# Optimization experiments

Measured on AMD Instinct MI355X. Metric: run time of the kernel, lower is better.

The kernel has to match this reference:

```python
import jax, jax.numpy as jnp
import numpy as np

B, S, E = 2, 2048, 2048
H, HKV = 16, 4
G = H // HKV
QLR, KVLR = 1024, 512
DN, DR, DV = 128, 64, 128
DQK = DN + DR
EPS = 1.1920929e-07  # torch.finfo(float32).eps, F.rms_norm default


def rms_norm(x):
    return x * jax.lax.rsqrt(jnp.mean(x * x, axis=-1, keepdims=True) + EPS)


def apply_rope(x, cos, sin):
    # x: [B, S, h, D]; pairs are adjacent elements (torch view_as_complex convention)
    x0, x1 = x[..., 0::2], x[..., 1::2]            # [B,S,h,D/2]
    c = cos[None, :, None, :]
    s = sin[None, :, None, :]
    r0 = x0 * c - x1 * s
    r1 = x0 * s + x1 * c
    return jnp.stack([r0, r1], axis=-1).reshape(x.shape)


def setup_inputs() -> dict:
    key = jax.random.key(0)
    ks = jax.random.split(key, 8)
    inv_freq = 1.0 / (10000.0 ** (np.arange(0, DR, 2, dtype=np.float32) / DR))  # [DR/2]
    ang = np.arange(S, dtype=np.float32)[:, None] * inv_freq[None, :]           # [S, DR/2]
    return {
        "x": jax.random.normal(ks[0], (B, S, E), jnp.float32),
        "freqs_cos": jnp.asarray(np.cos(ang), jnp.float32),
        "freqs_sin": jnp.asarray(np.sin(ang), jnp.float32),
        "Wqa": jax.random.normal(ks[1], (QLR, E), jnp.float32) * (E ** -0.5),
        "Wqb": jax.random.normal(ks[2], (H * DQK, QLR), jnp.float32) * (QLR ** -0.5),
        "Wkva": jax.random.normal(ks[3], (KVLR + DR, E), jnp.float32) * (E ** -0.5),
        "Wkvb": jax.random.normal(ks[4], (HKV * (DN + DV), KVLR), jnp.float32) * (KVLR ** -0.5),
        "Wo": jax.random.normal(ks[5], (E, H * DV), jnp.float32) * ((H * DV) ** -0.5),
    }


def reference(x, freqs_cos, freqs_sin, Wqa, Wqb, Wkva, Wkvb, Wo):
    # Q path: low-rank down-proj -> rmsnorm -> up-proj
    q = rms_norm(x @ Wqa.T) @ Wqb.T                       # [B,S,H*DQK]
    q = q.reshape(B, S, H, DQK)
    q_nope, q_rope = q[..., :DN], q[..., DN:]
    q_rope = apply_rope(q_rope, freqs_cos, freqs_sin)
    q = jnp.concatenate([q_nope, q_rope], axis=-1)        # [B,S,H,DQK]

    # KV path: joint down-proj, shared rope key, up-proj of latent
    kv_a = x @ Wkva.T                                     # [B,S,KVLR+DR]
    kv_latent, k_rope = kv_a[..., :KVLR], kv_a[..., KVLR:]
    k_rope = jnp.broadcast_to(k_rope[:, :, None, :], (B, S, HKV, DR))
    k_rope = apply_rope(k_rope, freqs_cos, freqs_sin)     # [B,S,HKV,DR]
    kv = (rms_norm(kv_latent) @ Wkvb.T).reshape(B, S, HKV, DN + DV)
    k_nope, v = kv[..., :DN], kv[..., DN:]
    k = jnp.concatenate([k_nope, k_rope], axis=-1)        # [B,S,HKV,DQK]

    # GQA causal SDPA: group G query heads per kv head
    qg = q.reshape(B, S, HKV, G, DQK)
    scores = jnp.einsum("bsngd,btnd->bngst", qg, k) * (DQK ** -0.5)  # [B,HKV,G,S,S]
    causal = jnp.tril(jnp.ones((S, S), bool))
    scores = jnp.where(causal, scores, jnp.finfo(scores.dtype).min)
    attn = jax.nn.softmax(scores, axis=-1)
    o = jnp.einsum("bngst,btnd->bsngd", attn, v).reshape(B, S, H * DV)
    return o @ Wo.T                                        # [B,S,E]
```

## Files before the change

### kernel.cpp

```cpp
#include <hip/hip_runtime.h>
#include <cstdint>
#include <cstddef>

typedef __attribute__((ext_vector_type(4))) float f32x4;
typedef __attribute__((ext_vector_type(2))) float f32x2;
typedef __attribute__((ext_vector_type(8))) short short8;
typedef __attribute__((ext_vector_type(8))) __bf16 bf16x8;
typedef unsigned short u16;
typedef unsigned int u32;
typedef __attribute__((ext_vector_type(2))) unsigned int u32x2;
typedef __attribute__((ext_vector_type(4))) unsigned short u16x4;
typedef __attribute__((ext_vector_type(2))) unsigned short u16x2;

#define EPS_RMS 1.1920929e-07f

__device__ __forceinline__ u16 f2bf(float f) {
  union { float f; unsigned u; } v; v.f = f;
  unsigned r = v.u + 0x7FFFu + ((v.u >> 16) & 1u);
  return (u16)(r >> 16);
}
__device__ __forceinline__ float b2f(u16 x) {
  union { unsigned u; float f; } v; v.u = ((unsigned)x) << 16;
  return v.f;
}
__device__ __forceinline__ u32 cvt_pk_bf16(float lo, float hi) {
  u32 r;
  asm("v_cvt_pk_bf16_f32 %0, %1, %2" : "=v"(r) : "v"(lo), "v"(hi));
  return r;
}

template <typename V>
__device__ __forceinline__ auto mfma_try(V a, V b, f32x4 c, int)
    -> decltype(__builtin_amdgcn_mfma_f32_16x16x32_bf16(a, b, c, 0, 0, 0)) {
  return __builtin_amdgcn_mfma_f32_16x16x32_bf16(a, b, c, 0, 0, 0);
}
template <typename V>
__device__ __forceinline__ f32x4 mfma_try(V a, V b, f32x4 c, long) {
  return __builtin_amdgcn_mfma_f32_16x16x32_bf16(
      __builtin_bit_cast(bf16x8, a), __builtin_bit_cast(bf16x8, b), c, 0, 0, 0);
}
__device__ __forceinline__ f32x4 mfma_bf16(short8 a, short8 b, f32x4 c) {
  return mfma_try(a, b, c, 0);
}

__device__ __forceinline__ void load_lds16(u16* lds, const u16* g) {
  auto* gp = reinterpret_cast<const __attribute__((address_space(1))) unsigned int*>(
      reinterpret_cast<uintptr_t>(g));
  auto* lp = reinterpret_cast<__attribute__((address_space(3))) unsigned int*>(
      reinterpret_cast<uintptr_t>(lds));
  __builtin_amdgcn_global_load_lds(gp, lp, 16, 0, 0);
}

__device__ __forceinline__ float fast_exp2(float x) {
  return __builtin_amdgcn_exp2f(x);
}

template <int CTRL>
__device__ __forceinline__ float dpp_step(float v) {
  int t = __builtin_amdgcn_update_dpp(0, __builtin_bit_cast(int, v), CTRL, 0xF, 0xF, true);
  return __builtin_bit_cast(float, t);
}

__global__ __launch_bounds__(256) void cvt_all(const float* __restrict__ x,
                                               const float* __restrict__ Wqa,
                                               const float* __restrict__ Wkva,
                                               const float* __restrict__ Wqb,
                                               const float* __restrict__ Wkvb,
                                               const float* __restrict__ Wo,
                                               u16* __restrict__ xb,
                                               u16* __restrict__ wacat,
                                               u16* __restrict__ wqb,
                                               u16* __restrict__ wkvb,
                                               u16* __restrict__ wo) {
  const int blk = blockIdx.x;
  if (blk >= 8192 && blk < 11520) {
    int i = (blk - 8192) * 256 + threadIdx.x;
    int r = i >> 9;
    int c4 = i & 511;
    f32x4 v = {0.f, 0.f, 0.f, 0.f};
    if (r < 1024) v = ((const f32x4*)Wqa)[r * 512 + c4];
    else if (r < 1600) v = ((const f32x4*)Wkva)[(r - 1024) * 512 + c4];
    u16x4 o = {f2bf(v.x), f2bf(v.y), f2bf(v.z), f2bf(v.w)};
    ((u16x4*)wacat)[i] = o;
    return;
  }
  const float* src;
  u16* dst;
  int i;
  if (blk < 8192)       { i = blk * 256 + threadIdx.x;           src = x;    dst = xb;   }
  else if (blk < 14592) { i = (blk - 11520) * 256 + threadIdx.x; src = Wqb;  dst = wqb;  }
  else if (blk < 15104) { i = (blk - 14592) * 256 + threadIdx.x; src = Wkvb; dst = wkvb; }
  else                  { i = (blk - 15104) * 256 + threadIdx.x; src = Wo;   dst = wo;   }
  f32x4 v = ((const f32x4*)src)[i];
  u16x4 o = {f2bf(v.x), f2bf(v.y), f2bf(v.z), f2bf(v.w)};
  ((u16x4*)dst)[i] = o;
}

template <typename OutT, int EPI>
__global__ __launch_bounds__(256) void gemm_bt(const u16* __restrict__ A,
                                               const u16* __restrict__ B,
                                               OutT* __restrict__ C,
                                               int M, int N, int K, int gx,
                                               const float* __restrict__ fc,
                                               const float* __restrict__ fs,
                                               u16* __restrict__ aux) {
  __shared__ __align__(16) u16 As[2][128 * 64];
  __shared__ __align__(16) u16 Bs[2][128 * 64];
  const int nwg = gridDim.x;
  const int cpx = nwg >> 3;
  const int swz = (blockIdx.x & 7) * cpx + (blockIdx.x >> 3);
  const int by = swz / gx, bxx = swz - by * gx;
  const int tid = threadIdx.x;
  const int lane = tid & 63, w = tid >> 6;
  const int wr = w >> 1, wc = w & 1;
  const int l16 = lane & 15, lg = lane >> 4;
  const int row0 = by * 128, col0 = bxx * 128;

  const u16* Ab = A + (size_t)row0 * K;
  const u16* Bb = B + (size_t)col0 * K;

  f32x4 acc[4][4] = {};

  int soff[4], ldst[4];
#pragma unroll
  for (int j = 0; j < 4; ++j) {
    int c = j * 256 + tid;
    int row = c >> 3;
    int rb = (c & 7) << 4;
    int sb = rb ^ ((row & 7) << 4);
    soff[j] = row * K + (sb >> 1);
    ldst[j] = c * 8;
  }

#pragma unroll
  for (int j = 0; j < 4; ++j) load_lds16(As[0] + ldst[j], Ab + soff[j]);
#pragma unroll
  for (int j = 0; j < 4; ++j) load_lds16(Bs[0] + ldst[j], Bb + soff[j]);
  __syncthreads();

  int cur = 0;
  for (int k0 = 0; k0 < K; k0 += 64) {
    if (k0 + 64 < K) {
#pragma unroll
      for (int j = 0; j < 4; ++j) load_lds16(As[cur ^ 1] + ldst[j], Ab + soff[j] + k0 + 64);
#pragma unroll
      for (int j = 0; j < 4; ++j) load_lds16(Bs[cur ^ 1] + ldst[j], Bb + soff[j] + k0 + 64);
    }
    const u16* Ac = As[cur];
    const u16* Bc = Bs[cur];
    short8 a[2][4], bfr[2][4];
#pragma unroll
    for (int mt = 0; mt < 4; ++mt) {
      const int rowA = wr * 64 + mt * 16 + l16;
      const int sw = (rowA & 7) << 4;
#pragma unroll
      for (int kk = 0; kk < 2; ++kk)
        a[kk][mt] = *(const short8*)(Ac + rowA * 64 + (((kk * 64 + lg * 16) ^ sw) >> 1));
    }
#pragma unroll
    for (int nt = 0; nt < 4; ++nt) {
      const int rowB = wc * 64 + nt * 16 + l16;
      const int sw = (rowB & 7) << 4;
#pragma unroll
      for (int kk = 0; kk < 2; ++kk)
        bfr[kk][nt] = *(const short8*)(Bc + rowB * 64 + (((kk * 64 + lg * 16) ^ sw) >> 1));
    }
#pragma unroll
    for (int kk = 0; kk < 2; ++kk)
#pragma unroll
      for (int mt = 0; mt < 4; ++mt)
#pragma unroll
        for (int nt = 0; nt < 4; ++nt)
          acc[mt][nt] = mfma_bf16(a[kk][mt], bfr[kk][nt], acc[mt][nt]);
    __syncthreads();
    cur ^= 1;
  }

  if constexpr (EPI == 0 || EPI == 1) {
#pragma unroll
    for (int mt = 0; mt < 4; ++mt)
#pragma unroll
      for (int nt = 0; nt < 4; ++nt)
#pragma unroll
        for (int i = 0; i < 4; ++i) {
          int row = row0 + wr * 64 + mt * 16 + lg * 4 + i;
          int col = col0 + wc * 64 + nt * 16 + l16;
          if constexpr (EPI == 0)
            C[(size_t)row * N + col] = acc[mt][nt][i];
          else
            C[(size_t)row * N + col] = f2bf(acc[mt][nt][i]);
        }
  } else if constexpr (EPI == 2) {
    const float qscale = 0.07216878364870322f * 1.4426950408889634f;
#pragma unroll
    for (int mt = 0; mt < 4; ++mt)
#pragma unroll
      for (int nt = 0; nt < 4; ++nt) {
        int col = col0 + wc * 64 + nt * 16 + l16;
        int hh = ((col >> 6) * 43) >> 7;
        int cin = col - hh * 192;
        int m = (cin - 128) >> 1;
#pragma unroll
        for (int i = 0; i < 4; ++i) {
          int row = row0 + wr * 64 + mt * 16 + lg * 4 + i;
          int bb = row >> 11, ss = row & 2047;
          float v = acc[mt][nt][i];
          float pv = dpp_step<0xB1>(v);
          float val = v;
          if (cin >= 128) {
            float c = fc[ss * 32 + m], sn = fs[ss * 32 + m];
            val = ((l16 & 1) == 0) ? (v * c - pv * sn) : (pv * sn + v * c);
          }
          ((u16*)C)[((size_t)((bb * 16 + hh) * 2048 + ss)) * 192 + cin] = f2bf(val * qscale);
        }
      }
  } else {
#pragma unroll
    for (int mt = 0; mt < 4; ++mt)
#pragma unroll
      for (int nt = 0; nt < 4; ++nt) {
        int col = col0 + wc * 64 + nt * 16 + l16;
        int nn = col >> 8, cin = col & 255;
        int rowb = row0 + wr * 64 + mt * 16 + lg * 4;
        int bb = rowb >> 11, ss0 = rowb & 2047;
        if (cin < 128) {
#pragma unroll
          for (int i = 0; i < 4; ++i)
            ((u16*)C)[((size_t)((bb * 4 + nn) * 2048 + ss0 + i)) * 192 + cin] =
                f2bf(acc[mt][nt][i]);
        } else {
          int dv = cin - 128;
          u16x4 o = {f2bf(acc[mt][nt][0]), f2bf(acc[mt][nt][1]),
                     f2bf(acc[mt][nt][2]), f2bf(acc[mt][nt][3])};
          *(u16x4*)(aux + ((size_t)((bb * 4 + nn) * 128 + dv)) * 2048 + ss0) = o;
        }
      }
  }
}

__global__ __launch_bounds__(256) void rms_fused(const u16* __restrict__ c1b,
                                                 const float* __restrict__ fc,
                                                 const float* __restrict__ fs,
                                                 u16* __restrict__ qlat,
                                                 u16* __restrict__ kvlat,
                                                 u16* __restrict__ Ka) {
  __shared__ float smq[4], smk[4];
  int t = blockIdx.x;
  const u16* row = c1b + (size_t)t * 1664;
  u16x4 v4u = ((const u16x4*)row)[threadIdx.x];
  u16x2 v2u = ((const u16x2*)(row + 1024))[threadIdx.x];
  float v4x = b2f(v4u.x), v4y = b2f(v4u.y), v4z = b2f(v4u.z), v4w = b2f(v4u.w);
  float v2x = b2f(v2u.x), v2y = b2f(v2u.y);
  float sq = v4x * v4x + v4y * v4y + v4z * v4z + v4w * v4w;
  float sk = v2x * v2x + v2y * v2y;
#pragma unroll
  for (int off = 32; off; off >>= 1) { sq += __shfl_xor(sq, off); sk += __shfl_xor(sk, off); }
  if ((threadIdx.x & 63) == 0) { smq[threadIdx.x >> 6] = sq; smk[threadIdx.x >> 6] = sk; }
  __syncthreads();
  float rq = rsqrtf((smq[0] + smq[1] + smq[2] + smq[3]) * (1.0f / 1024.0f) + EPS_RMS);
  float rk = rsqrtf((smk[0] + smk[1] + smk[2] + smk[3]) * (1.0f / 512.0f) + EPS_RMS);
  u16x4 oq = {f2bf(v4x * rq), f2bf(v4y * rq), f2bf(v4z * rq), f2bf(v4w * rq)};
  ((u16x4*)(qlat + (size_t)t * 1024))[threadIdx.x] = oq;
  u16x2 ok = {f2bf(v2x * rk), f2bf(v2y * rk)};
  ((u16x2*)(kvlat + (size_t)t * 512))[threadIdx.x] = ok;
  if (threadIdx.x < 32) {
    int bb = t >> 11, s = t & 2047;
    int m = threadIdx.x;
    float x0 = b2f(row[1536 + 2 * m]), x1 = b2f(row[1537 + 2 * m]);
    float c = fc[s * 32 + m], sn = fs[s * 32 + m];
    u16 r0 = f2bf(x0 * c - x1 * sn);
    u16 r1 = f2bf(x0 * sn + x1 * c);
#pragma unroll
    for (int nn = 0; nn < 4; ++nn) {
      size_t base = ((size_t)((bb * 4 + nn) * 2048 + s)) * 192 + 128;
      Ka[base + 2 * m] = r0;
      Ka[base + 2 * m + 1] = r1;
    }
  }
}

__global__ __launch_bounds__(256, 2) void attn_kernel(const u16* __restrict__ Qa,
                                                      const u16* __restrict__ Ka,
                                                      const u16* __restrict__ VTp,
                                                      u16* __restrict__ Ob) {
  __shared__ __align__(16) u16 Ks[64 * 192];
  __shared__ __align__(16) u16 Vs[128 * 64];
  __shared__ __align__(16) u32 Ppk[4][32][36];
  const int gid = blockIdx.x;
  const int bx = (gid < 256) ? (15 - (gid >> 5)) : ((gid - 256) >> 5);
  const int hb = gid & 31;
  const int b = hb >> 4;
  const int h = hb & 15;
  const int n = h >> 2;
  const int tid = threadIdx.x;
  const int lane = tid & 63;
  const int w = tid >> 6;
  const int l16 = lane & 15;
  const int lg = lane >> 4;

  const u16* Qp = Qa + ((size_t)((b * 16 + h) * 2048 + bx * 128 + w * 32)) * 192;
  const u16* Kp = Ka + ((size_t)((b * 4 + n) * 2048)) * 192;
  const u16* Vp = VTp + ((size_t)((b * 4 + n) * 128)) * 2048;

  int oK[6];
#pragma unroll
  for (int j = 0; j < 6; ++j) {
    int c = j * 256 + tid;
    int row = (c * 2731) >> 16;
    int rb = (c - row * 24) << 4;
    int sb = rb ^ ((row & 7) << 4);
    oK[j] = row * 192 + (sb >> 1);
  }
  int oV[4];
#pragma unroll
  for (int j = 0; j < 4; ++j) {
    int c = j * 256 + tid;
    int row = c >> 3;
    int rb = (c & 7) << 4;
    int sb = rb ^ ((row & 7) << 4);
    oV[j] = row * 2048 + (sb >> 1);
  }

  short8 qf[2][6];
#pragma unroll
  for (int g = 0; g < 2; ++g)
#pragma unroll
    for (int kc = 0; kc < 6; ++kc)
      qf[g][kc] = *(const short8*)(Qp + (size_t)(g * 16 + l16) * 192 + kc * 32 + lg * 8);

  float mrow[2], lrow[2];
  f32x4 oacc[2][8];
#pragma unroll
  for (int g = 0; g < 2; ++g) { mrow[g] = -1e30f; lrow[g] = 0.f; }
#pragma unroll
  for (int g = 0; g < 2; ++g)
#pragma unroll
    for (int vb = 0; vb < 8; ++vb) oacc[g][vb] = (f32x4){0.f, 0.f, 0.f, 0.f};

  const int wrow = bx * 128 + w * 32;
  const int NT = 2 * bx + 2;

  f32x4 kreg[6], vreg[4];
#pragma unroll
  for (int j = 0; j < 6; ++j) kreg[j] = *(const f32x4*)(Kp + oK[j]);
#pragma unroll
  for (int j = 0; j < 4; ++j) vreg[j] = *(const f32x4*)(Vp + oV[j]);

  for (int kt = 0; kt < NT; ++kt) {
    const int kb = kt * 64;
    __syncthreads();
#pragma unroll
    for (int j = 0; j < 6; ++j) *(f32x4*)(Ks + (j * 256 + tid) * 8) = kreg[j];
#pragma unroll
    for (int j = 0; j < 4; ++j) *(f32x4*)(Vs + (j * 256 + tid) * 8) = vreg[j];
    __syncthreads();
    if (kt + 1 < NT) {
      const int kb2 = kb + 64;
#pragma unroll
      for (int j = 0; j < 6; ++j)
        kreg[j] = *(const f32x4*)(Kp + oK[j] + (size_t)kb2 * 192);
#pragma unroll
      for (int j = 0; j < 4; ++j)
        vreg[j] = *(const f32x4*)(Vp + oV[j] + kb2);
    }
    if (kb > wrow + 31) continue;

    f32x4 sc[2][4];
#pragma unroll
    for (int g = 0; g < 2; ++g)
#pragma unroll
      for (int kn = 0; kn < 4; ++kn) sc[g][kn] = (f32x4){0.f, 0.f, 0.f, 0.f};
    __builtin_amdgcn_s_setprio(1);
#pragma unroll
    for (int kn = 0; kn < 4; ++kn) {
      const int rk = kn * 16 + l16;
      const u16* kbase = Ks + rk * 192;
      const int sw = (rk & 7) << 4;
#pragma unroll
      for (int kc = 0; kc < 6; ++kc) {
        short8 kf = *(const short8*)(kbase + (((kc * 64 + lg * 16) ^ sw) >> 1));
        sc[0][kn] = mfma_bf16(kf, qf[0][kc], sc[0][kn]);
        sc[1][kn] = mfma_bf16(kf, qf[1][kc], sc[1][kn]);
      }
    }
    __builtin_amdgcn_s_setprio(0);
    if (kb + 63 > wrow) {
#pragma unroll
      for (int g = 0; g < 2; ++g) {
        const int qabs = wrow + g * 16 + l16;
#pragma unroll
        for (int kn = 0; kn < 4; ++kn)
#pragma unroll
          for (int i = 0; i < 4; ++i)
            if (kb + kn * 16 + lg * 4 + i > qabs) sc[g][kn][i] = -1e30f;
      }
    }
    float pmax[2];
    int need = 0;
#pragma unroll
    for (int g = 0; g < 2; ++g) {
      float v = -1e30f;
#pragma unroll
      for (int kn = 0; kn < 4; ++kn)
        v = fmaxf(v, fmaxf(fmaxf(sc[g][kn][0], sc[g][kn][1]),
                           fmaxf(sc[g][kn][2], sc[g][kn][3])));
      v = fmaxf(v, __shfl_xor(v, 16));
      v = fmaxf(v, __shfl_xor(v, 32));
      pmax[g] = v;
      need |= (v > mrow[g] + 8.0f) ? 1 : 0;
    }
    if (__any(need)) {
#pragma unroll
      for (int g = 0; g < 2; ++g) {
        float mn = fmaxf(mrow[g], pmax[g]);
        float al = fast_exp2(mrow[g] - mn);
        mrow[g] = mn;
        lrow[g] *= al;
#pragma unroll
        for (int i = 0; i < 4; ++i) {
          float alq = __shfl(al, lg * 4 + i);
#pragma unroll
          for (int vb = 0; vb < 8; ++vb) oacc[g][vb][i] *= alq;
        }
      }
    }
#pragma unroll
    for (int g = 0; g < 2; ++g) {
      float rs = 0.f;
#pragma unroll
      for (int kn = 0; kn < 4; ++kn)
#pragma unroll
        for (int i = 0; i < 4; ++i) {
          float p = fast_exp2(sc[g][kn][i] - mrow[g]);
          sc[g][kn][i] = p;
          rs += p;
        }
      rs += __shfl_xor(rs, 16);
      rs += __shfl_xor(rs, 32);
      lrow[g] += rs;
    }
#pragma unroll
    for (int g = 0; g < 2; ++g) {
      const int r = g * 16 + l16;
#pragma unroll
      for (int kn = 0; kn < 4; ++kn) {
        u32x2 pk = {cvt_pk_bf16(sc[g][kn][0], sc[g][kn][1]),
                    cvt_pk_bf16(sc[g][kn][2], sc[g][kn][3])};
        *(u32x2*)&Ppk[w][r][kn * 8 + 2 * lg] = pk;
      }
    }
    short8 pa[2][2];
#pragma unroll
    for (int g = 0; g < 2; ++g) {
      const int r = g * 16 + l16;
      pa[g][0] = *(const short8*)&Ppk[w][r][lg * 4];
      pa[g][1] = *(const short8*)&Ppk[w][r][16 + lg * 4];
    }
    __builtin_amdgcn_s_setprio(1);
#pragma unroll
    for (int vb = 0; vb < 8; ++vb) {
      const int rv = vb * 16 + l16;
      const u16* vbase = Vs + rv * 64;
      const int swv = (rv & 7) << 4;
      short8 v0 = *(const short8*)(vbase + (((lg * 16) ^ swv) >> 1));
      short8 v1 = *(const short8*)(vbase + (((64 + lg * 16) ^ swv) >> 1));
      oacc[0][vb] = mfma_bf16(pa[0][0], v0, oacc[0][vb]);
      oacc[1][vb] = mfma_bf16(pa[1][0], v0, oacc[1][vb]);
      oacc[0][vb] = mfma_bf16(pa[0][1], v1, oacc[0][vb]);
      oacc[1][vb] = mfma_bf16(pa[1][1], v1, oacc[1][vb]);
    }
    __builtin_amdgcn_s_setprio(0);
  }
#pragma unroll
  for (int g = 0; g < 2; ++g) {
    float inv = 1.0f / lrow[g];
#pragma unroll
    for (int i = 0; i < 4; ++i) {
      float invq = __shfl(inv, lg * 4 + i);
      int srow = wrow + g * 16 + lg * 4 + i;
      size_t base = ((size_t)(b * 2048 + srow)) * 2048 + h * 128;
#pragma unroll
      for (int vb = 0; vb < 8; ++vb)
        Ob[base + vb * 16 + l16] = f2bf(oacc[g][vb][i] * invq);
    }
  }
}

extern "C" void kernel_launch(void* const* d_in, const int* in_sizes, int n_in,
                              void* d_out, int out_size, void* d_ws, size_t ws_size,
                              hipStream_t stream) {
  const float* x = (const float*)d_in[0];
  const float* fc = (const float*)d_in[1];
  const float* fs = (const float*)d_in[2];
  const float* Wqa = (const float*)d_in[3];
  const float* Wqb = (const float*)d_in[4];
  const float* Wkva = (const float*)d_in[5];
  const float* Wkvb = (const float*)d_in[6];
  const float* Wo = (const float*)d_in[7];
  float* out = (float*)d_out;

  char* ws = (char*)d_ws;
  u16* xb    = (u16*)(ws + 0);
  u16* wacat = (u16*)(ws + 16777216);
  u16* wqb   = (u16*)(ws + 23592960);
  u16* wkvb  = (u16*)(ws + 29884416);
  u16* wo    = (u16*)(ws + 30932992);
  u16* c1b   = (u16*)(ws + 39321600);
  u16* qlat  = (u16*)(ws + 52953088);
  u16* kvlat = (u16*)(ws + 61341696);
  u16* obf   = (u16*)(ws + 65536000);
  u16* qattn = (u16*)(ws + 82313216);
  u16* kattn = (u16*)(ws + 107479040);
  u16* vt    = (u16*)(ws + 113770496);
  if (ws_size < 117964800u) return;

  cvt_all<<<19200, 256, 0, stream>>>(x, Wqa, Wkva, Wqb, Wkvb, Wo,
                                     xb, wacat, wqb, wkvb, wo);

  gemm_bt<u16, 1><<<416, 256, 0, stream>>>(xb, wacat, c1b, 4096, 1664, 2048, 13,
                                           nullptr, nullptr, nullptr);
  rms_fused<<<4096, 256, 0, stream>>>(c1b, fc, fs, qlat, kvlat, kattn);
  gemm_bt<u16, 2><<<768, 256, 0, stream>>>(qlat, wqb, qattn, 4096, 3072, 1024, 24,
                                           fc, fs, nullptr);
  gemm_bt<u16, 3><<<256, 256, 0, stream>>>(kvlat, wkvb, kattn, 4096, 1024, 512, 8,
                                           nullptr, nullptr, vt);
  attn_kernel<<<512, 256, 0, stream>>>(qattn, kattn, vt, obf);
  gemm_bt<float, 0><<<512, 256, 0, stream>>>(obf, wo, out, 4096, 2048, 2048, 16,
                                             nullptr, nullptr, nullptr);
}
```

Baseline: 238.0 us.

## Double-buffer K/V tiles in LDS and drop to one barrier per iteration

```diff
diff --git a/kernel.cpp b/kernel.cpp
--- a/kernel.cpp
+++ b/kernel.cpp
@@ -283,9 +283,9 @@
                                                       const u16* __restrict__ Ka,
                                                       const u16* __restrict__ VTp,
                                                       u16* __restrict__ Ob) {
-  __shared__ __align__(16) u16 Ks[64 * 192];
-  __shared__ __align__(16) u16 Vs[128 * 64];
-  __shared__ __align__(16) u32 Ppk[4][32][36];
+  __shared__ __align__(16) u16 Ks[2][64 * 192];
+  __shared__ __align__(16) u16 Vs[2][128 * 64];
+  __shared__ __align__(16) u32 Ppk[4][16][36];
   const int gid = blockIdx.x;
   const int bx = (gid < 256) ? (15 - (gid >> 5)) : ((gid - 256) >> 5);
   const int hb = gid & 31;
@@ -345,17 +345,51 @@
   for (int j = 0; j < 6; ++j) kreg[j] = *(const f32x4*)(Kp + oK[j]);
 #pragma unroll
   for (int j = 0; j < 4; ++j) vreg[j] = *(const f32x4*)(Vp + oV[j]);
-
+#pragma unroll
+  for (int j = 0; j < 6; ++j) *(f32x4*)(Ks[0] + (j * 256 + tid) * 8) = kreg[j];
+#pragma unroll
+  for (int j = 0; j < 4; ++j) *(f32x4*)(Vs[0] + (j * 256 + tid) * 8) = vreg[j];
+#pragma unroll
+  for (int j = 0; j < 6; ++j) kreg[j] = *(const f32x4*)(Kp + oK[j] + (size_t)64 * 192);
+#pragma unroll
+  for (int j = 0; j < 4; ++j) vreg[j] = *(const f32x4*)(Vp + oV[j] + 64);
+  __syncthreads();
+
+  int cur = 0;
   for (int kt = 0; kt < NT; ++kt) {
     const int kb = kt * 64;
-    __syncthreads();
-#pragma unroll
-    for (int j = 0; j < 6; ++j) *(f32x4*)(Ks + (j * 256 + tid) * 8) = kreg[j];
-#pragma unroll
-    for (int j = 0; j < 4; ++j) *(f32x4*)(Vs + (j * 256 + tid) * 8) = vreg[j];
-    __syncthreads();
+    const bool act = (kb <= wrow + 31);
+
+    f32x4 sc[2][4];
+#pragma unroll
+    for (int g = 0; g < 2; ++g)
+#pragma unroll
+      for (int kn = 0; kn < 4; ++kn) sc[g][kn] = (f32x4){0.f, 0.f, 0.f, 0.f};
+    if (act) {
+      __builtin_amdgcn_s_setprio(1);
+#pragma unroll
+      for (int kn = 0; kn < 4; ++kn) {
+        const int rk = kn * 16 + l16;
+        const u16* kbase = Ks[cur] + rk * 192;
+        const int sw = (rk & 7) << 4;
+#pragma unroll
+        for (int kc = 0; kc < 6; ++kc) {
+          short8 kf = *(const short8*)(kbase + (((kc * 64 + lg * 16) ^ sw) >> 1));
+          sc[0][kn] = mfma_bf16(kf, qf[0][kc], sc[0][kn]);
+          sc[1][kn] = mfma_bf16(kf, qf[1][kc], sc[1][kn]);
+        }
+      }
+      __builtin_amdgcn_s_setprio(0);
+    }
+
     if (kt + 1 < NT) {
-      const int kb2 = kb + 64;
+#pragma unroll
+      for (int j = 0; j < 6; ++j) *(f32x4*)(Ks[cur ^ 1] + (j * 256 + tid) * 8) = kreg[j];
+#pragma unroll
+      for (int j = 0; j < 4; ++j) *(f32x4*)(Vs[cur ^ 1] + (j * 256 + tid) * 8) = vreg[j];
+    }
+    if (kt + 2 < NT) {
+      const int kb2 = (kt + 2) * 64;
 #pragma unroll
       for (int j = 0; j < 6; ++j)
         kreg[j] = *(const f32x4*)(Kp + oK[j] + (size_t)kb2 * 192);
@@ -363,113 +397,92 @@
       for (int j = 0; j < 4; ++j)
         vreg[j] = *(const f32x4*)(Vp + oV[j] + kb2);
     }
-    if (kb > wrow + 31) continue;
-
-    f32x4 sc[2][4];
-#pragma unroll
-    for (int g = 0; g < 2; ++g)
-#pragma unroll
-      for (int kn = 0; kn < 4; ++kn) sc[g][kn] = (f32x4){0.f, 0.f, 0.f, 0.f};
-    __builtin_amdgcn_s_setprio(1);
-#pragma unroll
-    for (int kn = 0; kn < 4; ++kn) {
-      const int rk = kn * 16 + l16;
-      const u16* kbase = Ks + rk * 192;
-      const int sw = (rk & 7) << 4;
-#pragma unroll
-      for (int kc = 0; kc < 6; ++kc) {
-        short8 kf = *(const short8*)(kbase + (((kc * 64 + lg * 16) ^ sw) >> 1));
-        sc[0][kn] = mfma_bf16(kf, qf[0][kc], sc[0][kn]);
-        sc[1][kn] = mfma_bf16(kf, qf[1][kc], sc[1][kn]);
-      }
-    }
-    __builtin_amdgcn_s_setprio(0);
-    if (kb + 63 > wrow) {
+
+    if (act) {
+      if (kb + 63 > wrow) {
+#pragma unroll
+        for (int g = 0; g < 2; ++g) {
+          const int qabs = wrow + g * 16 + l16;
+#pragma unroll
+          for (int kn = 0; kn < 4; ++kn)
+#pragma unroll
+            for (int i = 0; i < 4; ++i)
+              if (kb + kn * 16 + lg * 4 + i > qabs) sc[g][kn][i] = -1e30f;
+        }
+      }
+      float pmax[2];
+      int need = 0;
 #pragma unroll
       for (int g = 0; g < 2; ++g) {
-        const int qabs = wrow + g * 16 + l16;
+        float v = -1e30f;
 #pragma unroll
         for (int kn = 0; kn < 4; ++kn)
-#pragma unroll
-          for (int i = 0; i < 4; ++i)
-            if (kb + kn * 16 + lg * 4 + i > qabs) sc[g][kn][i] = -1e30f;
-      }
-    }
-    float pmax[2];
-    int need = 0;
-#pragma unroll
-    for (int g = 0; g < 2; ++g) {
-      float v = -1e30f;
-#pragma unroll
-      for (int kn = 0; kn < 4; ++kn)
-        v = fmaxf(v, fmaxf(fmaxf(sc[g][kn][0], sc[g][kn][1]),
-                           fmaxf(sc[g][kn][2], sc[g][kn][3])));
-      v = fmaxf(v, __shfl_xor(v, 16));
-      v = fmaxf(v, __shfl_xor(v, 32));
-      pmax[g] = v;
-      need |= (v > mrow[g] + 8.0f) ? 1 : 0;
-    }
-    if (__any(need)) {
+          v = fmaxf(v, fmaxf(fmaxf(sc[g][kn][0], sc[g][kn][1]),
+                             fmaxf(sc[g][kn][2], sc[g][kn][3])));
+        v = fmaxf(v, __shfl_xor(v, 16));
+        v = fmaxf(v, __shfl_xor(v, 32));
+        pmax[g] = v;
+        need |= (v > mrow[g] + 8.0f) ? 1 : 0;
+      }
+      if (__any(need)) {
+#pragma unroll
+        for (int g = 0; g < 2; ++g) {
+          float mn = fmaxf(mrow[g], pmax[g]);
+          float al = fast_exp2(mrow[g] - mn);
+          mrow[g] = mn;
+          lrow[g] *= al;
+#pragma unroll
+          for (int i = 0; i < 4; ++i) {
+            float alq = __shfl(al, lg * 4 + i);
+#pragma unroll
+            for (int vb = 0; vb < 8; ++vb) oacc[g][vb][i] *= alq;
+          }
+        }
+      }
 #pragma unroll
       for (int g = 0; g < 2; ++g) {
-        float mn = fmaxf(mrow[g], pmax[g]);
-        float al = fast_exp2(mrow[g] - mn);
-        mrow[g] = mn;
-        lrow[g] *= al;
-#pragma unroll
-        for (int i = 0; i < 4; ++i) {
-          float alq = __shfl(al, lg * 4 + i);
-#pragma unroll
-          for (int vb = 0; vb < 8; ++vb) oacc[g][vb][i] *= alq;
-        }
-      }
-    }
-#pragma unroll
-    for (int g = 0; g < 2; ++g) {
-      float rs = 0.f;
-#pragma unroll
-      for (int kn = 0; kn < 4; ++kn)
-#pragma unroll
-        for (int i = 0; i < 4; ++i) {
-          float p = fast_exp2(sc[g][kn][i] - mrow[g]);
-          sc[g][kn][i] = p;
-          rs += p;
-        }
-      rs += __shfl_xor(rs, 16);
-      rs += __shfl_xor(rs, 32);
-      lrow[g] += rs;
-    }
-#pragma unroll
-    for (int g = 0; g < 2; ++g) {
-      const int r = g * 16 + l16;
-#pragma unroll
-      for (int kn = 0; kn < 4; ++kn) {
-        u32x2 pk = {cvt_pk_bf16(sc[g][kn][0], sc[g][kn][1]),
-                    cvt_pk_bf16(sc[g][kn][2], sc[g][kn][3])};
-        *(u32x2*)&Ppk[w][r][kn * 8 + 2 * lg] = pk;
-      }
-    }
-    short8 pa[2][2];
-#pragma unroll
-    for (int g = 0; g < 2; ++g) {
-      const int r = g * 16 + l16;
-      pa[g][0] = *(const short8*)&Ppk[w][r][lg * 4];
-      pa[g][1] = *(const short8*)&Ppk[w][r][16 + lg * 4];
-    }
-    __builtin_amdgcn_s_setprio(1);
-#pragma unroll
-    for (int vb = 0; vb < 8; ++vb) {
-      const int rv = vb * 16 + l16;
-      const u16* vbase = Vs + rv * 64;
-      const int swv = (rv & 7) << 4;
-      short8 v0 = *(const short8*)(vbase + (((lg * 16) ^ swv) >> 1));
-      short8 v1 = *(const short8*)(vbase + (((64 + lg * 16) ^ swv) >> 1));
-      oacc[0][vb] = mfma_bf16(pa[0][0], v0, oacc[0][vb]);
-      oacc[1][vb] = mfma_bf16(pa[1][0], v0, oacc[1][vb]);
-      oacc[0][vb] = mfma_bf16(pa[0][1], v1, oacc[0][vb]);
-      oacc[1][vb] = mfma_bf16(pa[1][1], v1, oacc[1][vb]);
-    }
-    __builtin_amdgcn_s_setprio(0);
+        float rs = 0.f;
+#pragma unroll
+        for (int kn = 0; kn < 4; ++kn)
+#pragma unroll
+          for (int i = 0; i < 4; ++i) {
+            float p = fast_exp2(sc[g][kn][i] - mrow[g]);
+            sc[g][kn][i] = p;
+            rs += p;
+          }
+        rs += __shfl_xor(rs, 16);
+        rs += __shfl_xor(rs, 32);
+        lrow[g] += rs;
+      }
+      short8 pa[2][2];
+#pragma unroll
+      for (int g = 0; g < 2; ++g) {
+#pragma unroll
+        for (int kn = 0; kn < 4; ++kn) {
+          u32x2 pk = {cvt_pk_bf16(sc[g][kn][0], sc[g][kn][1]),
+                      cvt_pk_bf16(sc[g][kn][2], sc[g][kn][3])};
+          *(u32x2*)&Ppk[w][l16][kn * 8 + 2 * lg] = pk;
+        }
+        pa[g][0] = *(const short8*)&Ppk[w][l16][lg * 4];
+        pa[g][1] = *(const short8*)&Ppk[w][l16][16 + lg * 4];
+      }
+      __builtin_amdgcn_s_setprio(1);
+#pragma unroll
+      for (int vb = 0; vb < 8; ++vb) {
+        const int rv = vb * 16 + l16;
+        const u16* vbase = Vs[cur] + rv * 64;
+        const int swv = (rv & 7) << 4;
+        short8 v0 = *(const short8*)(vbase + (((lg * 16) ^ swv) >> 1));
+        short8 v1 = *(const short8*)(vbase + (((64 + lg * 16) ^ swv) >> 1));
+        oacc[0][vb] = mfma_bf16(pa[0][0], v0, oacc[0][vb]);
+        oacc[1][vb] = mfma_bf16(pa[1][0], v0, oacc[1][vb]);
+        oacc[0][vb] = mfma_bf16(pa[0][1], v1, oacc[0][vb]);
+        oacc[1][vb] = mfma_bf16(pa[1][1], v1, oacc[1][vb]);
+      }
+      __builtin_amdgcn_s_setprio(0);
+    }
+    __syncthreads();
+    cur ^= 1;
   }
 #pragma unroll
   for (int g = 0; g < 2; ++g) {
```

New measurement: 277.4 us. +16.5%, slower.
